# Optimization experiments

Hardware: AMD Instinct MI355X
Metric: run time of the kernel (lower is better)

## Reference

```python
import jax, jax.numpy as jnp
import numpy as np
from math import log, sqrt

B, S, D, H, L = 16, 512, 512, 8, 6
DPH = D // H
DFF = 2048
VOCAB = 1024
MAXDEG = 64
NPC, NS = 4096, 4096


def setup_inputs() -> dict:
    rng = np.random.default_rng(0)
    raw_x = rng.integers(0, VOCAB + 1, (B, S)).astype(np.int32)
    scatter_degree = rng.integers(0, MAXDEG + 1, (B, S)).astype(np.int32)

    def uniq_triples(n, seed):
        r = np.random.default_rng(seed)
        flat = r.choice(B * S * S, n, replace=False)  # unique (b,i,j)
        b, i, j = np.unravel_index(flat, (B, S, S))
        return np.stack([b, i, j], 1).astype(np.int32)

    parentchild_indices = uniq_triples(NPC, 1)
    silbing_indices = uniq_triples(NS, 2)
    parent_child_now = np.stack([np.arange(B), rng.integers(0, S, B)], 1).astype(np.int32)
    silbing_now = np.stack([np.arange(B), rng.integers(0, S, B)], 1).astype(np.int32)

    key = jax.random.key(0)
    ks = jax.random.split(key, 16)
    sc = 0.02
    inp = {
        "raw_x": jnp.asarray(raw_x),
        "scatter_degree": jnp.asarray(scatter_degree),
        "parentchild_indices": jnp.asarray(parentchild_indices),
        "parent_child_now": jnp.asarray(parent_child_now),
        "silbing_indices": jnp.asarray(silbing_indices),
        "silbing_now": jnp.asarray(silbing_now),
        "vocab_emb": jax.random.normal(ks[0], (VOCAB + 1, D), jnp.float32) * sc,
        "degree_emb": jax.random.normal(ks[1], (MAXDEG + 1, D), jnp.float32) * sc,
        "active_rel_emb": jax.random.normal(ks[2], (2, D), jnp.float32) * sc,
        "relation_encoder": jax.random.uniform(ks[3], (3,), jnp.float32),
        "Wq": jax.random.normal(ks[4], (L, D, D), jnp.float32) * sc,
        "bq": jnp.zeros((L, D), jnp.float32),
        "Wk": jax.random.normal(ks[5], (L, D, D), jnp.float32) * sc,
        "bk": jnp.zeros((L, D), jnp.float32),
        "Wv": jax.random.normal(ks[6], (L, D, D), jnp.float32) * sc,
        "bv": jnp.zeros((L, D), jnp.float32),
        "Wo": jax.random.normal(ks[7], (L, D, D), jnp.float32) * sc,
        "bo": jnp.zeros((L, D), jnp.float32),
        "W1": jax.random.normal(ks[8], (L, DFF, D), jnp.float32) * sc,
        "b1": jnp.zeros((L, DFF), jnp.float32),
        "W2": jax.random.normal(ks[9], (L, D, DFF), jnp.float32) * sc,
        "b2": jnp.zeros((L, D), jnp.float32),
        "ln_g": jnp.ones((L, D), jnp.float32),
        "ln_b": jnp.zeros((L, D), jnp.float32),
        "logits_w": jax.random.normal(ks[10], (VOCAB, D), jnp.float32) * sc,
    }
    return inp


def _layer_norm(x, g, b):
    m = jnp.mean(x, -1, keepdims=True)
    v = jnp.mean((x - m) ** 2, -1, keepdims=True)  # biased var, eps=1e-5 (torch default)
    return (x - m) * jax.lax.rsqrt(v + 1e-5) * g + b


def _forward(raw_x, scatter_degree, parentchild_indices, parent_child_now,
             silbing_indices, silbing_now, vocab_emb, degree_emb, active_rel_emb,
             relation_encoder, Wq, bq, Wk, bk, Wv, bv, Wo, bo, W1, b1, W2, b2,
             ln_g, ln_b, logits_w):
    x = vocab_emb[raw_x]  # [B,S,D]
    # sinusoidal positional encoding
    pos = jnp.arange(S, dtype=jnp.float32)[:, None]
    div = jnp.exp(jnp.arange(0, D, 2, dtype=jnp.float32) * (-log(10000.0) / D))
    pe = jnp.zeros((S, D), x.dtype).at[:, 0::2].set(jnp.sin(pos * div)).at[:, 1::2].set(jnp.cos(pos * div))
    x = x + pe
    # structural encodings
    x = x + degree_emb[scatter_degree]
    x = x.at[parent_child_now[:, 0], parent_child_now[:, 1]].add(active_rel_emb[0])
    x = x.at[silbing_now[:, 0], silbing_now[:, 1]].add(active_rel_emb[1])

    pb, pi, pj = parentchild_indices[:, 0], parentchild_indices[:, 1], parentchild_indices[:, 2]
    sb, si, sj = silbing_indices[:, 0], silbing_indices[:, 1], silbing_indices[:, 2]
    inv_norm = 1.0 / sqrt(DPH)

    for l in range(L):
        q = (x @ Wq[l].T + bq[l]).reshape(B, S, H, DPH).transpose(0, 2, 1, 3)
        k = (x @ Wk[l].T + bk[l]).reshape(B, S, H, DPH).transpose(0, 2, 1, 3)
        v = (x @ Wv[l].T + bv[l]).reshape(B, S, H, DPH).transpose(0, 2, 1, 3)
        scores = jnp.einsum('bhqd,bhkd->bhqk', q, k) * inv_norm  # [B,H,S,S]
        # scatter-added relational bias (broadcast over all heads)
        scores = scores.at[pb, :, pi, pj].add(relation_encoder[0])
        scores = scores.at[pb, :, pj, pi].add(relation_encoder[1])
        scores = scores.at[sb, :, si, sj].add(relation_encoder[2])
        scores = scores.at[sb, :, sj, si].add(relation_encoder[2])
        attn = jax.nn.softmax(scores, axis=-1)
        o = jnp.einsum('bhqk,bhkd->bhqd', attn, v).transpose(0, 2, 1, 3).reshape(B, S, D)
        o = o @ Wo[l].T + bo[l]
        x = _layer_norm(x + o, ln_g[l], ln_b[l])
        ff = jax.nn.relu(x @ W1[l].T + b1[l]) @ W2[l].T + b2[l]
        x = _layer_norm(x + ff, ln_g[l], ln_b[l])

    return x[:, -1] @ logits_w.T  # [B, VOCAB]


def reference(raw_x, scatter_degree, parentchild_indices, parent_child_now,
              silbing_indices, silbing_now, vocab_emb, degree_emb, active_rel_emb,
              relation_encoder, Wq, bq, Wk, bk, Wv, bv, Wo, bo, W1, b1, W2, b2,
              ln_g, ln_b, logits_w):
    return _forward(raw_x, scatter_degree, parentchild_indices, parent_child_now,
                    silbing_indices, silbing_now, vocab_emb, degree_emb, active_rel_emb,
                    relation_encoder, Wq, bq, Wk, bk, Wv, bv, Wo, bo, W1, b1, W2, b2,
                    ln_g, ln_b, logits_w)
```

## Files before the change

### kernel.cpp

```cpp
#include <hip/hip_runtime.h>
#include <hip/hip_bf16.h>
#include <math.h>

#define B_ 16
#define S_ 512
#define D_ 512
#define H_ 8
#define L_ 6
#define DPH_ 64
#define DFF_ 2048
#define VOCAB_ 1024
#define NPC_ 4096
#define NS_ 4096
#define BS_ (B_ * S_)
#define LOG2E 1.4426950408889634f

typedef __attribute__((ext_vector_type(8))) short bf16x8;
typedef __attribute__((ext_vector_type(4))) float f32x4;

__device__ __forceinline__ ushort f2bf(float f) {
    __hip_bfloat16 h = __float2bfloat16(f);
    return __builtin_bit_cast(ushort, h);
}
__device__ __forceinline__ float bf2f(ushort u) {
    unsigned int v = ((unsigned int)u) << 16;
    return __builtin_bit_cast(float, v);
}

__global__ __launch_bounds__(256) void embed_kernel(
    const int* __restrict__ raw_x, const int* __restrict__ sdeg,
    const float* __restrict__ vemb, const float* __restrict__ demb,
    ushort* __restrict__ xb)
{
    size_t idx = (size_t)blockIdx.x * 256 + threadIdx.x;
    int d = (int)(idx & (D_ - 1));
    size_t bs = idx >> 9;
    int s = (int)(bs & (S_ - 1));
    int tok = raw_x[bs];
    int dg  = sdeg[bs];
    float e = expf(-(float)(d & ~1) * (9.210340371976184f / (float)D_));
    float ang = (float)s * e;
    float pe = (d & 1) ? cosf(ang) : sinf(ang);
    xb[idx] = f2bf(vemb[(size_t)tok * D_ + d] + pe + demb[(size_t)dg * D_ + d]);
}

__global__ void relnow_kernel(const int* __restrict__ pcn, const int* __restrict__ sbn,
                              const float* __restrict__ arel, ushort* __restrict__ xb)
{
    int b = blockIdx.x;
    int t = threadIdx.x;
    int b1 = pcn[b * 2 + 0], p1 = pcn[b * 2 + 1];
    size_t i1 = ((size_t)(b1 * S_ + p1)) * D_ + t;
    xb[i1] = f2bf(bf2f(xb[i1]) + arel[t]);
    int b2 = sbn[b * 2 + 0], p2 = sbn[b * 2 + 1];
    size_t i2 = ((size_t)(b2 * S_ + p2)) * D_ + t;
    xb[i2] = f2bf(bf2f(xb[i2]) + arel[D_ + t]);
}

__global__ void bias_scatter_kernel(const int* __restrict__ pc, const int* __restrict__ sb,
                                    const float* __restrict__ renc, float* __restrict__ bias)
{
    int t = blockIdx.x * 256 + threadIdx.x;
    float r0 = renc[0], r1 = renc[1], r2 = renc[2];
    if (t < NPC_) {
        int b = pc[t * 3 + 0], i = pc[t * 3 + 1], j = pc[t * 3 + 2];
        atomicAdd(&bias[((size_t)b * S_ + i) * S_ + j], r0);
        atomicAdd(&bias[((size_t)b * S_ + j) * S_ + i], r1);
    } else if (t < NPC_ + NS_) {
        int u = t - NPC_;
        int b = sb[u * 3 + 0], i = sb[u * 3 + 1], j = sb[u * 3 + 2];
        atomicAdd(&bias[((size_t)b * S_ + i) * S_ + j], r2);
        atomicAdd(&bias[((size_t)b * S_ + j) * S_ + i], r2);
    }
}

__global__ __launch_bounds__(256) void bias_cast_kernel(const float* __restrict__ src,
                                                        ushort* __restrict__ dst)
{
    int i = blockIdx.x * 256 + threadIdx.x;
    float4 v = ((const float4*)src)[i];
    ushort4 o;
    o.x = f2bf(v.x * LOG2E); o.y = f2bf(v.y * LOG2E);
    o.z = f2bf(v.z * LOG2E); o.w = f2bf(v.w * LOG2E);
    ((ushort4*)dst)[i] = o;
}

__global__ __launch_bounds__(256) void cast4_kernel(const float* __restrict__ src,
                                                    ushort* __restrict__ dst, int n4)
{
    int i = blockIdx.x * 256 + threadIdx.x;
    if (i >= n4) return;
    float4 v = ((const float4*)src)[i];
    ushort4 o;
    o.x = f2bf(v.x); o.y = f2bf(v.y); o.z = f2bf(v.z); o.w = f2bf(v.w);
    ((ushort4*)dst)[i] = o;
}

__global__ __launch_bounds__(256) void pack_qkv_kernel(
    const float* __restrict__ Wq, const float* __restrict__ Wk, const float* __restrict__ Wv,
    ushort* __restrict__ dst)
{
    int idx = blockIdx.x * 256 + threadIdx.x;
    int c = idx & 511;
    int rl = idx >> 9;
    int r = rl % 1536, l = rl / 1536;
    float v;
    if (r < 512)       v = Wq[((size_t)l * 512 + r) * 512 + c];
    else if (r < 1024) v = Wk[((size_t)l * 512 + (r - 512)) * 512 + c];
    else               v = Wv[((size_t)l * 512 + (r - 1024)) * 512 + c];
    dst[idx] = f2bf(v);
}

__global__ void pack_bqkv_kernel(const float* __restrict__ bq, const float* __restrict__ bk,
                                 const float* __restrict__ bv, float* __restrict__ dst)
{
    int idx = blockIdx.x * 256 + threadIdx.x;
    if (idx >= L_ * 1536) return;
    int r = idx % 1536, l = idx / 1536;
    float v;
    if (r < 512)       v = bq[l * 512 + r];
    else if (r < 1024) v = bk[l * 512 + r - 512];
    else               v = bv[l * 512 + r - 1024];
    dst[idx] = v;
}

#define GL2LDS(g, l) __builtin_amdgcn_global_load_lds( \
    (const __attribute__((address_space(1))) void*)(g), \
    (__attribute__((address_space(3))) void*)(l), 16, 0, 0)

__global__ __launch_bounds__(256) void gemm_bf16(
    const ushort* __restrict__ A, const ushort* __restrict__ W,
    const float* __restrict__ bias, ushort* __restrict__ Cb,
    int K, int M, int mode)
{
    __shared__ ushort As0[128 * 32];
    __shared__ ushort As1[128 * 32];
    __shared__ ushort Bs0[128 * 32];
    __shared__ ushort Bs1[128 * 32];

    const int t  = threadIdx.x;
    const int wv = t >> 6;
    const int ln = t & 63;
    const int wm = wv >> 1, wn = wv & 1;
    const int lq = ln >> 4, lc = ln & 15;
    const int row0 = blockIdx.x * 128;
    const int col0 = blockIdx.y * 128;
    const int lr = ln >> 2;
    const int lk = (ln & 3) * 8;

    f32x4 acc[4][4] = {};

    for (int k0 = 0; k0 < K; k0 += 64) {
        #pragma unroll
        for (int i = 0; i < 2; i++) {
            int r = i * 64 + wv * 16;
            const ushort* ga = A + (size_t)(row0 + r + lr) * K + k0 + lk;
            const ushort* gb = W + (size_t)(col0 + r + lr) * K + k0 + lk;
            GL2LDS(ga,      &As0[r * 32]);
            GL2LDS(gb,      &Bs0[r * 32]);
            GL2LDS(ga + 32, &As1[r * 32]);
            GL2LDS(gb + 32, &Bs1[r * 32]);
        }
        __syncthreads();

        bf16x8 af[4], bf[4];
        #pragma unroll
        for (int mi = 0; mi < 4; mi++)
            af[mi] = *(const bf16x8*)&As0[(wm * 64 + mi * 16 + lc) * 32 + lq * 8];
        #pragma unroll
        for (int ni = 0; ni < 4; ni++)
            bf[ni] = *(const bf16x8*)&Bs0[(wn * 64 + ni * 16 + lc) * 32 + lq * 8];
        #pragma unroll
        for (int mi = 0; mi < 4; mi++)
            #pragma unroll
            for (int ni = 0; ni < 4; ni++)
                acc[mi][ni] = __builtin_amdgcn_mfma_f32_16x16x32_bf16(af[mi], bf[ni], acc[mi][ni], 0, 0, 0);

        #pragma unroll
        for (int mi = 0; mi < 4; mi++)
            af[mi] = *(const bf16x8*)&As1[(wm * 64 + mi * 16 + lc) * 32 + lq * 8];
        #pragma unroll
        for (int ni = 0; ni < 4; ni++)
            bf[ni] = *(const bf16x8*)&Bs1[(wn * 64 + ni * 16 + lc) * 32 + lq * 8];
        #pragma unroll
        for (int mi = 0; mi < 4; mi++)
            #pragma unroll
            for (int ni = 0; ni < 4; ni++)
                acc[mi][ni] = __builtin_amdgcn_mfma_f32_16x16x32_bf16(af[mi], bf[ni], acc[mi][ni], 0, 0, 0);
        __syncthreads();
    }

    #pragma unroll
    for (int mi = 0; mi < 4; mi++) {
        #pragma unroll
        for (int ni = 0; ni < 4; ni++) {
            int gcol = col0 + wn * 64 + ni * 16 + lc;
            float bb = bias[gcol];
            #pragma unroll
            for (int rr = 0; rr < 4; rr++) {
                int grow = row0 + wm * 64 + mi * 16 + lq * 4 + rr;
                float val = acc[mi][ni][rr] + bb;
                if (mode == 1) val = fmaxf(val, 0.f);
                Cb[(size_t)grow * M + gcol] = f2bf(val);
            }
        }
    }
}

__global__ __launch_bounds__(256) void gemm64(
    const ushort* __restrict__ A, const ushort* __restrict__ W,
    ushort* __restrict__ Cb, int K, int M)
{
    __shared__ ushort As0[128 * 32];
    __shared__ ushort As1[128 * 32];
    __shared__ ushort Bs0[64 * 32];
    __shared__ ushort Bs1[64 * 32];

    const int t  = threadIdx.x;
    const int wv = t >> 6;
    const int ln = t & 63;
    const int wm = wv >> 1, wn = wv & 1;
    const int lq = ln >> 4, lc = ln & 15;
    const int row0 = blockIdx.x * 128;
    const int col0 = blockIdx.y * 64;
    const int lr = ln >> 2;
    const int lk = (ln & 3) * 8;

    f32x4 acc[4][2] = {};

    for (int k0 = 0; k0 < K; k0 += 64) {
        #pragma unroll
        for (int i = 0; i < 2; i++) {
            int r = i * 64 + wv * 16;
            const ushort* ga = A + (size_t)(row0 + r + lr) * K + k0 + lk;
            GL2LDS(ga,      &As0[r * 32]);
            GL2LDS(ga + 32, &As1[r * 32]);
        }
        {
            int rb = wv * 16;
            const ushort* gb = W + (size_t)(col0 + rb + lr) * K + k0 + lk;
            GL2LDS(gb,      &Bs0[rb * 32]);
            GL2LDS(gb + 32, &Bs1[rb * 32]);
        }
        __syncthreads();

        bf16x8 af[4], bf[2];
        #pragma unroll
        for (int mi = 0; mi < 4; mi++)
            af[mi] = *(const bf16x8*)&As0[(wm * 64 + mi * 16 + lc) * 32 + lq * 8];
        #pragma unroll
        for (int ni = 0; ni < 2; ni++)
            bf[ni] = *(const bf16x8*)&Bs0[(wn * 32 + ni * 16 + lc) * 32 + lq * 8];
        #pragma unroll
        for (int mi = 0; mi < 4; mi++)
            #pragma unroll
            for (int ni = 0; ni < 2; ni++)
                acc[mi][ni] = __builtin_amdgcn_mfma_f32_16x16x32_bf16(af[mi], bf[ni], acc[mi][ni], 0, 0, 0);

        #pragma unroll
        for (int mi = 0; mi < 4; mi++)
            af[mi] = *(const bf16x8*)&As1[(wm * 64 + mi * 16 + lc) * 32 + lq * 8];
        #pragma unroll
        for (int ni = 0; ni < 2; ni++)
            bf[ni] = *(const bf16x8*)&Bs1[(wn * 32 + ni * 16 + lc) * 32 + lq * 8];
        #pragma unroll
        for (int mi = 0; mi < 4; mi++)
            #pragma unroll
            for (int ni = 0; ni < 2; ni++)
                acc[mi][ni] = __builtin_amdgcn_mfma_f32_16x16x32_bf16(af[mi], bf[ni], acc[mi][ni], 0, 0, 0);
        __syncthreads();
    }

    #pragma unroll
    for (int mi = 0; mi < 4; mi++)
        #pragma unroll
        for (int ni = 0; ni < 2; ni++) {
            int gcol = col0 + wn * 32 + ni * 16 + lc;
            #pragma unroll
            for (int rr = 0; rr < 4; rr++) {
                int grow = row0 + wm * 64 + mi * 16 + lq * 4 + rr;
                Cb[(size_t)grow * M + gcol] = f2bf(acc[mi][ni][rr]);
            }
        }
}

#define PSTR 72

__device__ __forceinline__ int vswz(int d, int j) {
    int g = ((j >> 3) ^ (d & 7) ^ ((d >> 3) & 7)) & 7;
    return d * 64 + g * 8 + (j & 7);
}

__global__ __launch_bounds__(256) void attn_kernel(
    const ushort* __restrict__ qkv, const ushort* __restrict__ biasb,
    ushort* __restrict__ ao)
{
    const int qt = blockIdx.x, h = blockIdx.y, b = blockIdx.z;
    const int t  = threadIdx.x;
    const int wq = t >> 6;
    const int ln = t & 63;
    const int lq = ln >> 4;
    const int lc = ln & 15;
    const int r  = t >> 2;
    const int cg = t & 3;

    __shared__ ushort Qs[64 * PSTR];
    __shared__ ushort Ks[64 * PSTR];
    __shared__ ushort Ps[64 * PSTR];
    __shared__ ushort Vts[64 * 64];

    const int i0 = qt * 64;

    {
        const ushort* qsrc = qkv + (size_t)(b * S_ + i0 + r) * 1536 + h * 64 + cg * 16;
        *(uint4*)&Qs[r * PSTR + cg * 16]     = ((const uint4*)qsrc)[0];
        *(uint4*)&Qs[r * PSTR + cg * 16 + 8] = ((const uint4*)qsrc)[1];
    }
    bf16x8 aq0 = *(const bf16x8*)&Qs[(wq * 16 + lc) * PSTR + lq * 8];
    bf16x8 aq1 = *(const bf16x8*)&Qs[(wq * 16 + lc) * PSTR + 32 + lq * 8];

    f32x4 of[4] = {};
    float l_lane[4] = {};
    const float QSC = 0.125f * LOG2E;

    for (int j0 = 0; j0 < S_; j0 += 64) {
        __syncthreads();
        {
            const ushort* ksrc = qkv + (size_t)(b * S_ + j0 + r) * 1536 + 512 + h * 64 + cg * 16;
            *(uint4*)&Ks[r * PSTR + cg * 16]     = ((const uint4*)ksrc)[0];
            *(uint4*)&Ks[r * PSTR + cg * 16 + 8] = ((const uint4*)ksrc)[1];
            const ushort* vsrc = ksrc + 512;
            ushort vv[16];
            *(uint4*)&vv[0] = ((const uint4*)vsrc)[0];
            *(uint4*)&vv[8] = ((const uint4*)vsrc)[1];
            #pragma unroll
            for (int dd = 0; dd < 16; dd++)
                Vts[vswz(cg * 16 + dd, r)] = vv[dd];
        }
        __syncthreads();

        f32x4 sf[4] = {};
        #pragma unroll
        for (int ni = 0; ni < 4; ni++) {
            bf16x8 bk0 = *(const bf16x8*)&Ks[(ni * 16 + lc) * PSTR + lq * 8];
            bf16x8 bk1 = *(const bf16x8*)&Ks[(ni * 16 + lc) * PSTR + 32 + lq * 8];
            sf[ni] = __builtin_amdgcn_mfma_f32_16x16x32_bf16(aq0, bk0, sf[ni], 0, 0, 0);
            sf[ni] = __builtin_amdgcn_mfma_f32_16x16x32_bf16(aq1, bk1, sf[ni], 0, 0, 0);
        }

        const ushort* bbase = biasb + (size_t)(b * S_ + i0 + wq * 16 + lq * 4) * S_ + j0;
        #pragma unroll
        for (int ni = 0; ni < 4; ni++)
            #pragma unroll
            for (int rr = 0; rr < 4; rr++) {
                float bv = bf2f(bbase[(size_t)rr * S_ + ni * 16 + lc]);
                float p = __builtin_amdgcn_exp2f(fmaf(sf[ni][rr], QSC, bv));
                l_lane[rr] += p;
                Ps[(wq * 16 + lq * 4 + rr) * PSTR + ni * 16 + lc] = f2bf(p);
            }

        bf16x8 ap0 = *(const bf16x8*)&Ps[(wq * 16 + lc) * PSTR + lq * 8];
        bf16x8 ap1 = *(const bf16x8*)&Ps[(wq * 16 + lc) * PSTR + 32 + lq * 8];
        #pragma unroll
        for (int ni = 0; ni < 4; ni++) {
            bf16x8 bv0 = *(const bf16x8*)&Vts[vswz(ni * 16 + lc, lq * 8)];
            bf16x8 bv1 = *(const bf16x8*)&Vts[vswz(ni * 16 + lc, 32 + lq * 8)];
            of[ni] = __builtin_amdgcn_mfma_f32_16x16x32_bf16(ap0, bv0, of[ni], 0, 0, 0);
            of[ni] = __builtin_amdgcn_mfma_f32_16x16x32_bf16(ap1, bv1, of[ni], 0, 0, 0);
        }
    }

    float inv[4];
    #pragma unroll
    for (int rr = 0; rr < 4; rr++) {
        float s = l_lane[rr];
        s += __shfl_xor(s, 1);
        s += __shfl_xor(s, 2);
        s += __shfl_xor(s, 4);
        s += __shfl_xor(s, 8);
        inv[rr] = 1.f / s;
    }
    #pragma unroll
    for (int ni = 0; ni < 4; ni++)
        #pragma unroll
        for (int rr = 0; rr < 4; rr++) {
            int row = i0 + wq * 16 + lq * 4 + rr;
            ao[(size_t)(b * S_ + row) * D_ + h * 64 + ni * 16 + lc] = f2bf(of[ni][rr] * inv[rr]);
        }
}

__device__ __forceinline__ float block_sum(float v, float* red) {
    #pragma unroll
    for (int off = 32; off > 0; off >>= 1) v += __shfl_down(v, off);
    int t = threadIdx.x;
    if ((t & 63) == 0) red[t >> 6] = v;
    __syncthreads();
    float r = red[0] + red[1] + red[2] + red[3];
    __syncthreads();
    return r;
}

__global__ __launch_bounds__(256) void add_ln_kernel(
    ushort* __restrict__ xb, const ushort* __restrict__ pb,
    const float* __restrict__ bvec,
    const float* __restrict__ g, const float* __restrict__ bta)
{
    __shared__ float red[4];
    const int row = blockIdx.x;
    const int t = threadIdx.x;
    const size_t base = (size_t)row * D_;
    float v0 = bf2f(xb[base + t])       + bf2f(pb[base + t])       + bvec[t];
    float v1 = bf2f(xb[base + t + 256]) + bf2f(pb[base + t + 256]) + bvec[t + 256];
    float mean = block_sum(v0 + v1, red) * (1.f / (float)D_);
    float d0 = v0 - mean, d1 = v1 - mean;
    float var = block_sum(d0 * d0 + d1 * d1, red) * (1.f / (float)D_);
    float inv = rsqrtf(var + 1e-5f);
    float o0 = d0 * inv * g[t] + bta[t];
    float o1 = d1 * inv * g[t + 256] + bta[t + 256];
    xb[base + t]       = f2bf(o0);
    xb[base + t + 256] = f2bf(o1);
}

__global__ __launch_bounds__(256) void logits_kernel(
    const ushort* __restrict__ xb, const float* __restrict__ lw, float* __restrict__ out)
{
    __shared__ float xs[D_];
    const int b = blockIdx.x;
    const int vchunk = blockIdx.y;
    const int t = threadIdx.x;
    const ushort* xrow = xb + ((size_t)(b * S_ + (S_ - 1)) * D_);
    xs[t] = bf2f(xrow[t]);
    xs[t + 256] = bf2f(xrow[t + 256]);
    __syncthreads();
    for (int vv = vchunk * 128 + t; vv < vchunk * 128 + 128; vv += 256) {
        const float* wr = lw + (size_t)vv * D_;
        float acc = 0.f;
        #pragma unroll 8
        for (int d = 0; d < D_; d += 4) {
            float4 w4 = *(const float4*)&wr[d];
            acc += xs[d] * w4.x + xs[d + 1] * w4.y + xs[d + 2] * w4.z + xs[d + 3] * w4.w;
        }
        out[(size_t)b * VOCAB_ + vv] = acc;
    }
}

extern "C" void kernel_launch(void* const* d_in, const int* in_sizes, int n_in,
                              void* d_out, int out_size, void* d_ws, size_t ws_size,
                              hipStream_t stream)
{
    const int* raw_x = (const int*)d_in[0];
    const int* sdeg  = (const int*)d_in[1];
    const int* pci   = (const int*)d_in[2];
    const int* pcn   = (const int*)d_in[3];
    const int* sbi   = (const int*)d_in[4];
    const int* sbn   = (const int*)d_in[5];
    const float* vemb = (const float*)d_in[6];
    const float* demb = (const float*)d_in[7];
    const float* arel = (const float*)d_in[8];
    const float* renc = (const float*)d_in[9];
    const float* Wq = (const float*)d_in[10];
    const float* bq = (const float*)d_in[11];
    const float* Wk = (const float*)d_in[12];
    const float* bk = (const float*)d_in[13];
    const float* Wv = (const float*)d_in[14];
    const float* bv = (const float*)d_in[15];
    const float* Wo = (const float*)d_in[16];
    const float* bo = (const float*)d_in[17];
    const float* W1 = (const float*)d_in[18];
    const float* b1 = (const float*)d_in[19];
    const float* W2 = (const float*)d_in[20];
    const float* b2 = (const float*)d_in[21];
    const float* lng = (const float*)d_in[22];
    const float* lnb = (const float*)d_in[23];
    const float* lw  = (const float*)d_in[24];
    float* out = (float*)d_out;

    float* wsf = (float*)d_ws;
    const size_t X = (size_t)BS_ * D_;
    ushort* xb   = (ushort*)wsf;
    ushort* qkvb = (ushort*)(wsf + X / 2);
    ushort* ao   = (ushort*)(wsf + 2 * X);
    ushort* h1   = (ushort*)(wsf + (X * 5) / 2);
    ushort* projb= (ushort*)(wsf + (X * 9) / 2);
    float*  bias = wsf + 5 * X;
    ushort* biasb= (ushort*)(wsf + 6 * X);
    ushort* wb   = (ushort*)(wsf + (X * 13) / 2);
    ushort* wqkv_b = wb;
    ushort* wo_b   = wb + 4718592;
    ushort* w1_b   = wb + 6291456;
    ushort* w2_b   = wb + 12582912;
    float*  bqkv   = wsf + (X * 13) / 2 + 9437184;

    embed_kernel<<<(B_ * S_ * D_) / 256, 256, 0, stream>>>(raw_x, sdeg, vemb, demb, xb);
    relnow_kernel<<<B_, D_, 0, stream>>>(pcn, sbn, arel, xb);

    hipMemsetAsync(bias, 0, (size_t)B_ * S_ * S_ * sizeof(float), stream);
    bias_scatter_kernel<<<(NPC_ + NS_ + 255) / 256, 256, 0, stream>>>(pci, sbi, renc, bias);
    bias_cast_kernel<<<(B_ * S_ * S_ / 4) / 256, 256, 0, stream>>>(bias, biasb);

    pack_qkv_kernel<<<(L_ * 1536 * 512) / 256, 256, 0, stream>>>(Wq, Wk, Wv, wqkv_b);
    pack_bqkv_kernel<<<(L_ * 1536 + 255) / 256, 256, 0, stream>>>(bq, bk, bv, bqkv);
    cast4_kernel<<<(L_ * 512 * 512) / 4 / 256, 256, 0, stream>>>(Wo, wo_b, L_ * 512 * 512 / 4);
    cast4_kernel<<<(L_ * 2048 * 512) / 4 / 256, 256, 0, stream>>>(W1, w1_b, L_ * 2048 * 512 / 4);
    cast4_kernel<<<(L_ * 512 * 2048) / 4 / 256, 256, 0, stream>>>(W2, w2_b, L_ * 512 * 2048 / 4);

    dim3 blk(256);
    for (int l = 0; l < L_; l++) {
        gemm_bf16<<<dim3(BS_ / 128, 1536 / 128), blk, 0, stream>>>(
            xb, wqkv_b + (size_t)l * 1536 * 512, bqkv + l * 1536, qkvb, 512, 1536, 2);

        attn_kernel<<<dim3(S_ / 64, H_, B_), blk, 0, stream>>>(qkvb, biasb, ao);

        gemm64<<<dim3(BS_ / 128, 512 / 64), blk, 0, stream>>>(
            ao, wo_b + (size_t)l * 512 * 512, projb, 512, 512);
        add_ln_kernel<<<BS_, blk, 0, stream>>>(xb, projb, bo + l * 512,
                                               lng + l * D_, lnb + l * D_);

        gemm_bf16<<<dim3(BS_ / 128, 2048 / 128), blk, 0, stream>>>(
            xb, w1_b + (size_t)l * 2048 * 512, b1 + l * 2048, h1, 512, 2048, 1);
        gemm64<<<dim3(BS_ / 128, 512 / 64), blk, 0, stream>>>(
            h1, w2_b + (size_t)l * 512 * 2048, projb, 2048, 512);
        add_ln_kernel<<<BS_, blk, 0, stream>>>(xb, projb, b2 + l * 512,
                                               lng + l * D_, lnb + l * D_);
    }

    logits_kernel<<<dim3(B_, 8), blk, 0, stream>>>(xb, lw, out);
}
```

Before: 1.082 ms.

## Double-buffer GEMM k-tiles and stage two key blocks per attention iteration

```diff
diff --git a/kernel.cpp b/kernel.cpp
--- a/kernel.cpp
+++ b/kernel.cpp
@@ -128,6 +128,29 @@
     (const __attribute__((address_space(1))) void*)(g), \
     (__attribute__((address_space(3))) void*)(l), 16, 0, 0)
 
+#define STAGE_AB(AsX, BsX, kk) do {                                            \
+    _Pragma("unroll")                                                          \
+    for (int i_ = 0; i_ < 2; i_++) {                                           \
+        int r_ = i_ * 64 + wv * 16;                                            \
+        GL2LDS(A + (size_t)(row0 + r_ + lr) * K + (kk) + lk, &AsX[r_ * 32]);   \
+        GL2LDS(W + (size_t)(col0 + r_ + lr) * K + (kk) + lk, &BsX[r_ * 32]);   \
+    } } while (0)
+
+#define COMPUTE_AB(AsX, BsX) do {                                              \
+    bf16x8 af[4], bf[4];                                                       \
+    _Pragma("unroll")                                                          \
+    for (int mi = 0; mi < 4; mi++)                                             \
+        af[mi] = *(const bf16x8*)&AsX[(wm * 64 + mi * 16 + lc) * 32 + lq * 8]; \
+    _Pragma("unroll")                                                          \
+    for (int ni = 0; ni < 4; ni++)                                             \
+        bf[ni] = *(const bf16x8*)&BsX[(wn * 64 + ni * 16 + lc) * 32 + lq * 8]; \
+    _Pragma("unroll")                                                          \
+    for (int mi = 0; mi < 4; mi++)                                             \
+        _Pragma("unroll")                                                      \
+        for (int ni = 0; ni < 4; ni++)                                         \
+            acc[mi][ni] = __builtin_amdgcn_mfma_f32_16x16x32_bf16(af[mi], bf[ni], acc[mi][ni], 0, 0, 0); \
+    } while (0)
+
 __global__ __launch_bounds__(256) void gemm_bf16(
     const ushort* __restrict__ A, const ushort* __restrict__ W,
     const float* __restrict__ bias, ushort* __restrict__ Cb,
@@ -149,45 +172,16 @@
     const int lk = (ln & 3) * 8;
 
     f32x4 acc[4][4] = {};
-
-    for (int k0 = 0; k0 < K; k0 += 64) {
-        #pragma unroll
-        for (int i = 0; i < 2; i++) {
-            int r = i * 64 + wv * 16;
-            const ushort* ga = A + (size_t)(row0 + r + lr) * K + k0 + lk;
-            const ushort* gb = W + (size_t)(col0 + r + lr) * K + k0 + lk;
-            GL2LDS(ga,      &As0[r * 32]);
-            GL2LDS(gb,      &Bs0[r * 32]);
-            GL2LDS(ga + 32, &As1[r * 32]);
-            GL2LDS(gb + 32, &Bs1[r * 32]);
-        }
+    const int nk = K >> 5;
+
+    STAGE_AB(As0, Bs0, 0);
+    for (int ki = 0; ki < nk; ki += 2) {
         __syncthreads();
-
-        bf16x8 af[4], bf[4];
-        #pragma unroll
-        for (int mi = 0; mi < 4; mi++)
-            af[mi] = *(const bf16x8*)&As0[(wm * 64 + mi * 16 + lc) * 32 + lq * 8];
-        #pragma unroll
-        for (int ni = 0; ni < 4; ni++)
-            bf[ni] = *(const bf16x8*)&Bs0[(wn * 64 + ni * 16 + lc) * 32 + lq * 8];
-        #pragma unroll
-        for (int mi = 0; mi < 4; mi++)
-            #pragma unroll
-            for (int ni = 0; ni < 4; ni++)
-                acc[mi][ni] = __builtin_amdgcn_mfma_f32_16x16x32_bf16(af[mi], bf[ni], acc[mi][ni], 0, 0, 0);
-
-        #pragma unroll
-        for (int mi = 0; mi < 4; mi++)
-            af[mi] = *(const bf16x8*)&As1[(wm * 64 + mi * 16 + lc) * 32 + lq * 8];
-        #pragma unroll
-        for (int ni = 0; ni < 4; ni++)
-            bf[ni] = *(const bf16x8*)&Bs1[(wn * 64 + ni * 16 + lc) * 32 + lq * 8];
-        #pragma unroll
-        for (int mi = 0; mi < 4; mi++)
-            #pragma unroll
-            for (int ni = 0; ni < 4; ni++)
-                acc[mi][ni] = __builtin_amdgcn_mfma_f32_16x16x32_bf16(af[mi], bf[ni], acc[mi][ni], 0, 0, 0);
+        if (ki + 1 < nk) STAGE_AB(As1, Bs1, (ki + 1) << 5);
+        COMPUTE_AB(As0, Bs0);
         __syncthreads();
+        if (ki + 2 < nk) STAGE_AB(As0, Bs0, (ki + 2) << 5);
+        COMPUTE_AB(As1, Bs1);
     }
 
     #pragma unroll
@@ -207,6 +201,32 @@
     }
 }
 
+#define STAGE_A64(AsX, BsX, kk) do {                                           \
+    _Pragma("unroll")                                                          \
+    for (int i_ = 0; i_ < 2; i_++) {                                           \
+        int r_ = i_ * 64 + wv * 16;                                            \
+        GL2LDS(A + (size_t)(row0 + r_ + lr) * K + (kk) + lk, &AsX[r_ * 32]);   \
+    }                                                                          \
+    {                                                                          \
+        int rb_ = wv * 16;                                                     \
+        GL2LDS(W + (size_t)(col0 + rb_ + lr) * K + (kk) + lk, &BsX[rb_ * 32]); \
+    } } while (0)
+
+#define COMPUTE_A64(AsX, BsX) do {                                             \
+    bf16x8 af[4], bf[2];                                                       \
+    _Pragma("unroll")                                                          \
+    for (int mi = 0; mi < 4; mi++)                                             \
+        af[mi] = *(const bf16x8*)&AsX[(wm * 64 + mi * 16 + lc) * 32 + lq * 8]; \
+    _Pragma("unroll")                                                          \
+    for (int ni = 0; ni < 2; ni++)                                             \
+        bf[ni] = *(const bf16x8*)&BsX[(wn * 32 + ni * 16 + lc) * 32 + lq * 8]; \
+    _Pragma("unroll")                                                          \
+    for (int mi = 0; mi < 4; mi++)                                             \
+        _Pragma("unroll")                                                      \
+        for (int ni = 0; ni < 2; ni++)                                         \
+            acc[mi][ni] = __builtin_amdgcn_mfma_f32_16x16x32_bf16(af[mi], bf[ni], acc[mi][ni], 0, 0, 0); \
+    } while (0)
+
 __global__ __launch_bounds__(256) void gemm64(
     const ushort* __restrict__ A, const ushort* __restrict__ W,
     ushort* __restrict__ Cb, int K, int M)
@@ -227,48 +247,16 @@
     const int lk = (ln & 3) * 8;
 
     f32x4 acc[4][2] = {};
-
-    for (int k0 = 0; k0 < K; k0 += 64) {
-        #pragma unroll
-        for (int i = 0; i < 2; i++) {
-            int r = i * 64 + wv * 16;
-            const ushort* ga = A + (size_t)(row0 + r + lr) * K + k0 + lk;
-            GL2LDS(ga,      &As0[r * 32]);
-            GL2LDS(ga + 32, &As1[r * 32]);
-        }
-        {
-            int rb = wv * 16;
-            const ushort* gb = W + (size_t)(col0 + rb + lr) * K + k0 + lk;
-            GL2LDS(gb,      &Bs0[rb * 32]);
-            GL2LDS(gb + 32, &Bs1[rb * 32]);
-        }
+    const int nk = K >> 5;
+
+    STAGE_A64(As0, Bs0, 0);
+    for (int ki = 0; ki < nk; ki += 2) {
         __syncthreads();
-
-        bf16x8 af[4], bf[2];
-        #pragma unroll
-        for (int mi = 0; mi < 4; mi++)
-            af[mi] = *(const bf16x8*)&As0[(wm * 64 + mi * 16 + lc) * 32 + lq * 8];
-        #pragma unroll
-        for (int ni = 0; ni < 2; ni++)
-            bf[ni] = *(const bf16x8*)&Bs0[(wn * 32 + ni * 16 + lc) * 32 + lq * 8];
-        #pragma unroll
-        for (int mi = 0; mi < 4; mi++)
-            #pragma unroll
-            for (int ni = 0; ni < 2; ni++)
-                acc[mi][ni] = __builtin_amdgcn_mfma_f32_16x16x32_bf16(af[mi], bf[ni], acc[mi][ni], 0, 0, 0);
-
-        #pragma unroll
-        for (int mi = 0; mi < 4; mi++)
-            af[mi] = *(const bf16x8*)&As1[(wm * 64 + mi * 16 + lc) * 32 + lq * 8];
-        #pragma unroll
-        for (int ni = 0; ni < 2; ni++)
-            bf[ni] = *(const bf16x8*)&Bs1[(wn * 32 + ni * 16 + lc) * 32 + lq * 8];
-        #pragma unroll
-        for (int mi = 0; mi < 4; mi++)
-            #pragma unroll
-            for (int ni = 0; ni < 2; ni++)
-                acc[mi][ni] = __builtin_amdgcn_mfma_f32_16x16x32_bf16(af[mi], bf[ni], acc[mi][ni], 0, 0, 0);
+        if (ki + 1 < nk) STAGE_A64(As1, Bs1, (ki + 1) << 5);
+        COMPUTE_A64(As0, Bs0);
         __syncthreads();
+        if (ki + 2 < nk) STAGE_A64(As0, Bs0, (ki + 2) << 5);
+        COMPUTE_A64(As1, Bs1);
     }
 
     #pragma unroll
@@ -291,6 +279,35 @@
     return d * 64 + g * 8 + (j & 7);
 }
 
+#define ATTN_SUB(KsX, VtsX, jbase) do {                                        \
+    f32x4 sf[4] = {};                                                          \
+    _Pragma("unroll")                                                          \
+    for (int ni = 0; ni < 4; ni++) {                                           \
+        bf16x8 bk0 = *(const bf16x8*)&KsX[(ni * 16 + lc) * PSTR + lq * 8];     \
+        bf16x8 bk1 = *(const bf16x8*)&KsX[(ni * 16 + lc) * PSTR + 32 + lq * 8];\
+        sf[ni] = __builtin_amdgcn_mfma_f32_16x16x32_bf16(aq0, bk0, sf[ni], 0, 0, 0); \
+        sf[ni] = __builtin_amdgcn_mfma_f32_16x16x32_bf16(aq1, bk1, sf[ni], 0, 0, 0); \
+    }                                                                          \
+    const ushort* bbase = biasb + (size_t)(b * S_ + i0 + wq * 16 + lq * 4) * S_ + (jbase); \
+    _Pragma("unroll")                                                          \
+    for (int ni = 0; ni < 4; ni++)                                             \
+        _Pragma("unroll")                                                      \
+        for (int rr = 0; rr < 4; rr++) {                                       \
+            float bv = bf2f(bbase[(size_t)rr * S_ + ni * 16 + lc]);            \
+            float p = __builtin_amdgcn_exp2f(fmaf(sf[ni][rr], QSC, bv));       \
+            l_lane[rr] += p;                                                   \
+            Ps[(wq * 16 + lq * 4 + rr) * PSTR + ni * 16 + lc] = f2bf(p);       \
+        }                                                                      \
+    bf16x8 ap0 = *(const bf16x8*)&Ps[(wq * 16 + lc) * PSTR + lq * 8];          \
+    bf16x8 ap1 = *(const bf16x8*)&Ps[(wq * 16 + lc) * PSTR + 32 + lq * 8];     \
+    _Pragma("unroll")                                                          \
+    for (int ni = 0; ni < 4; ni++) {                                           \
+        bf16x8 bv0 = *(const bf16x8*)&VtsX[vswz(ni * 16 + lc, lq * 8)];        \
+        bf16x8 bv1 = *(const bf16x8*)&VtsX[vswz(ni * 16 + lc, 32 + lq * 8)];   \
+        of[ni] = __builtin_amdgcn_mfma_f32_16x16x32_bf16(ap0, bv0, of[ni], 0, 0, 0); \
+        of[ni] = __builtin_amdgcn_mfma_f32_16x16x32_bf16(ap1, bv1, of[ni], 0, 0, 0); \
+    } } while (0)
+
 __global__ __launch_bounds__(256) void attn_kernel(
     const ushort* __restrict__ qkv, const ushort* __restrict__ biasb,
     ushort* __restrict__ ao)
@@ -305,9 +322,11 @@
     const int cg = t & 3;
 
     __shared__ ushort Qs[64 * PSTR];
-    __shared__ ushort Ks[64 * PSTR];
+    __shared__ ushort Ks0[64 * PSTR];
+    __shared__ ushort Ks1[64 * PSTR];
     __shared__ ushort Ps[64 * PSTR];
-    __shared__ ushort Vts[64 * 64];
+    __shared__ ushort Vts0[64 * 64];
+    __shared__ ushort Vts1[64 * 64];
 
     const int i0 = qt * 64;
 
@@ -323,51 +342,31 @@
     float l_lane[4] = {};
     const float QSC = 0.125f * LOG2E;
 
-    for (int j0 = 0; j0 < S_; j0 += 64) {
+    for (int j0 = 0; j0 < S_; j0 += 128) {
         __syncthreads();
         {
-            const ushort* ksrc = qkv + (size_t)(b * S_ + j0 + r) * 1536 + 512 + h * 64 + cg * 16;
-            *(uint4*)&Ks[r * PSTR + cg * 16]     = ((const uint4*)ksrc)[0];
-            *(uint4*)&Ks[r * PSTR + cg * 16 + 8] = ((const uint4*)ksrc)[1];
-            const ushort* vsrc = ksrc + 512;
+            const ushort* ksrc0 = qkv + (size_t)(b * S_ + j0 + r) * 1536 + 512 + h * 64 + cg * 16;
+            const ushort* ksrc1 = ksrc0 + (size_t)64 * 1536;
+            *(uint4*)&Ks0[r * PSTR + cg * 16]     = ((const uint4*)ksrc0)[0];
+            *(uint4*)&Ks0[r * PSTR + cg * 16 + 8] = ((const uint4*)ksrc0)[1];
+            *(uint4*)&Ks1[r * PSTR + cg * 16]     = ((const uint4*)ksrc1)[0];
+            *(uint4*)&Ks1[r * PSTR + cg * 16 + 8] = ((const uint4*)ksrc1)[1];
             ushort vv[16];
-            *(uint4*)&vv[0] = ((const uint4*)vsrc)[0];
-            *(uint4*)&vv[8] = ((const uint4*)vsrc)[1];
+            *(uint4*)&vv[0] = ((const uint4*)(ksrc0 + 512))[0];
+            *(uint4*)&vv[8] = ((const uint4*)(ksrc0 + 512))[1];
             #pragma unroll
             for (int dd = 0; dd < 16; dd++)
-                Vts[vswz(cg * 16 + dd, r)] = vv[dd];
+                Vts0[vswz(cg * 16 + dd, r)] = vv[dd];
+            *(uint4*)&vv[0] = ((const uint4*)(ksrc1 + 512))[0];
+            *(uint4*)&vv[8] = ((const uint4*)(ksrc1 + 512))[1];
+            #pragma unroll
+            for (int dd = 0; dd < 16; dd++)
+                Vts1[vswz(cg * 16 + dd, r)] = vv[dd];
         }
         __syncthreads();
 
-        f32x4 sf[4] = {};
-        #pragma unroll
-        for (int ni = 0; ni < 4; ni++) {
-            bf16x8 bk0 = *(const bf16x8*)&Ks[(ni * 16 + lc) * PSTR + lq * 8];
-            bf16x8 bk1 = *(const bf16x8*)&Ks[(ni * 16 + lc) * PSTR + 32 + lq * 8];
-            sf[ni] = __builtin_amdgcn_mfma_f32_16x16x32_bf16(aq0, bk0, sf[ni], 0, 0, 0);
-            sf[ni] = __builtin_amdgcn_mfma_f32_16x16x32_bf16(aq1, bk1, sf[ni], 0, 0, 0);
-        }
-
-        const ushort* bbase = biasb + (size_t)(b * S_ + i0 + wq * 16 + lq * 4) * S_ + j0;
-        #pragma unroll
-        for (int ni = 0; ni < 4; ni++)
-            #pragma unroll
-            for (int rr = 0; rr < 4; rr++) {
-                float bv = bf2f(bbase[(size_t)rr * S_ + ni * 16 + lc]);
-                float p = __builtin_amdgcn_exp2f(fmaf(sf[ni][rr], QSC, bv));
-                l_lane[rr] += p;
-                Ps[(wq * 16 + lq * 4 + rr) * PSTR + ni * 16 + lc] = f2bf(p);
-            }
-
-        bf16x8 ap0 = *(const bf16x8*)&Ps[(wq * 16 + lc) * PSTR + lq * 8];
-        bf16x8 ap1 = *(const bf16x8*)&Ps[(wq * 16 + lc) * PSTR + 32 + lq * 8];
-        #pragma unroll
-        for (int ni = 0; ni < 4; ni++) {
-            bf16x8 bv0 = *(const bf16x8*)&Vts[vswz(ni * 16 + lc, lq * 8)];
-            bf16x8 bv1 = *(const bf16x8*)&Vts[vswz(ni * 16 + lc, 32 + lq * 8)];
-            of[ni] = __builtin_amdgcn_mfma_f32_16x16x32_bf16(ap0, bv0, of[ni], 0, 0, 0);
-            of[ni] = __builtin_amdgcn_mfma_f32_16x16x32_bf16(ap1, bv1, of[ni], 0, 0, 0);
-        }
+        ATTN_SUB(Ks0, Vts0, j0);
+        ATTN_SUB(Ks1, Vts1, j0 + 64);
     }
 
     float inv[4];
```

New measurement: 1.030 ms. 1.05x faster.
